# Optimization experiments

Hardware: AMD Instinct MI355X
Metric: run time of the kernel (lower is better)

The kernel has to match this reference:

```python
import jax, jax.numpy as jnp
import numpy as np

AGENT_RADIUS = 0.5
SAFETY_DIST = 0.1
QP_ITERS = 300


def _qp_solve(p, G, h):
    """Batched QP: min_u 0.5 u^T u + p^T u  s.t.  G u <= h  (Q = I).
    Solved in the dual by projected gradient ascent (differentiable, fixed iters).
    p: [B,2], G: [B,m,2], h: [B,m] -> u: [B,2]
    """
    GGt = jnp.einsum('bmi,bni->bmn', G, G)                 # [B,m,m]
    q = jnp.einsum('bmi,bi->bm', G, p) + h                 # [B,m]
    # Lipschitz upper bound per sample (Frobenius norm of GG^T)
    L = jnp.sqrt(jnp.sum(GGt * GGt, axis=(1, 2))) + 1e-6   # [B]
    alpha = (1.0 / L)[:, None]

    def step(lam, _):
        grad = jnp.einsum('bmn,bn->bm', GGt, lam) + q
        lam = jnp.maximum(lam - alpha * grad, 0.0)
        return lam, None

    lam0 = jnp.zeros_like(h)
    lam, _ = jax.lax.scan(step, lam0, None, length=QP_ITERS)
    u = -p - jnp.einsum('bmi,bm->bi', G, lam)
    return u


def setup_inputs() -> dict:
    key = jax.random.key(0)
    ks = jax.random.split(key, 20)
    B, F, H1, H2 = 8192, 8, 1024, 512

    def w(k, i, o):
        return (jax.random.normal(k, (i, o), jnp.float32) / np.sqrt(i)).astype(jnp.float32)

    obs_xy = jax.random.uniform(ks[17], (8, 2), jnp.float32, -10.0, 10.0)
    obs_r = jax.random.uniform(ks[18], (8, 1), jnp.float32, 0.3, 0.8)
    return {
        'x': jax.random.normal(ks[0], (B, F), jnp.float32),
        'mean': 0.1 * jax.random.normal(ks[1], (F,), jnp.float32),
        'std': jax.random.uniform(ks[2], (F,), jnp.float32, 0.5, 1.5),
        'W1': w(ks[3], F, H1), 'b1': jnp.zeros((H1,), jnp.float32),
        'W21': w(ks[4], H1, H2), 'b21': jnp.zeros((H2,), jnp.float32),
        'W22': w(ks[5], H1, H2), 'b22': jnp.zeros((H2,), jnp.float32),
        'W23': w(ks[6], H1, H2), 'b23': jnp.zeros((H2,), jnp.float32),
        'W31': w(ks[7], H2, 2), 'b31': jnp.zeros((2,), jnp.float32),
        'W32': w(ks[8], H2, 2), 'b32': jnp.zeros((2,), jnp.float32),
        'W33': w(ks[9], H2, 1), 'b33': jnp.zeros((1,), jnp.float32),
        'obstacles': jnp.concatenate([obs_xy, obs_r], axis=1),  # [8,3] (x,y,r)
        'sgn': 1,
    }


def reference(x, mean, std, W1, b1, W21, b21, W22, b22, W23, b23,
              W31, b31, W32, b32, W33, b33, obstacles, sgn):
    B = x.shape[0]
    x0 = x * std + mean                                   # un-normalized state [B,8]

    h1 = jax.nn.relu(x @ W1 + b1)
    x21 = jax.nn.relu(h1 @ W21 + b21)
    x22 = jax.nn.relu(h1 @ W22 + b22)
    x23 = jax.nn.relu(h1 @ W23 + b23)
    x31 = x21 @ W31 + b31                                 # QP linear term p [B,2]
    x32 = 4.0 * jax.nn.sigmoid(x22 @ W32 + b32)           # CBF gains p1,p2 [B,2]
    x33 = 4.0 * jax.nn.sigmoid(x23 @ W33 + b33)           # liveness gain (unused, smg off)

    px, py, theta, v = x0[:, 0], x0[:, 1], x0[:, 2], x0[:, 3]
    st, ct = jnp.sin(theta)[:, None], jnp.cos(theta)[:, None]
    vb = v[:, None]

    # static obstacles broadcast to batch + opponent as last obstacle -> [B, m]
    ox = jnp.concatenate([jnp.broadcast_to(obstacles[:, 0][None], (B, obstacles.shape[0])), x0[:, 4:5]], axis=1)
    oy = jnp.concatenate([jnp.broadcast_to(obstacles[:, 1][None], (B, obstacles.shape[0])), x0[:, 5:6]], axis=1)
    orad = jnp.concatenate([jnp.broadcast_to(obstacles[:, 2][None], (B, obstacles.shape[0])),
                            jnp.full((B, 1), AGENT_RADIUS, x0.dtype)], axis=1)

    R = AGENT_RADIUS + orad + SAFETY_DIST
    dx = px[:, None] - ox                                  # [B,m]
    dy = py[:, None] - oy

    barrier = dx * dx + dy * dy - R * R
    barrier_dot = 2.0 * dx * vb * ct + 2.0 * dy * vb * st
    Lf2b = (2.0 * v * v)[:, None]
    LgLfbu1 = -2.0 * dx * vb * st + 2.0 * dy * vb * ct
    LgLfbu2 = 2.0 * dx * ct + 2.0 * dy * st
    G = jnp.stack([-LgLfbu1, -LgLfbu2], axis=-1)           # [B,m,2]
    p1, p2 = x32[:, 0:1], x32[:, 1:2]
    h = Lf2b + (p1 + p2) * barrier_dot + p1 * p2 * barrier # [B,m]

    u = _qp_solve(x31, G, h)                               # [B,2]
    return u
```

## Files before the change

kernel.cpp:

```cpp
#include <hip/hip_runtime.h>
#include <cstdint>
#include <cstddef>

typedef unsigned short u16;
typedef u16   u16x8  __attribute__((ext_vector_type(8)));
typedef u16   u16x4  __attribute__((ext_vector_type(4)));
typedef __bf16 bf16x8 __attribute__((ext_vector_type(8)));
typedef float f32x4  __attribute__((ext_vector_type(4)));
typedef float f32x2  __attribute__((ext_vector_type(2)));

__device__ __forceinline__ u16 f2bf(float f) {
  unsigned int x = __builtin_bit_cast(unsigned int, f);
  x += 0x7fffu + ((x >> 16) & 1u);
  return (u16)(x >> 16);
}

__device__ __forceinline__ void gld_lds16(const u16* g, u16* l) {
  __builtin_amdgcn_global_load_lds(
      (const __attribute__((address_space(1))) unsigned int*)g,
      (__attribute__((address_space(3))) unsigned int*)l, 16, 0, 0);
}

__global__ __launch_bounds__(256) void k_prep(const float* __restrict__ W21,
                                              const float* __restrict__ W22,
                                              u16* __restrict__ Wt,
                                              const float* __restrict__ x,
                                              const float* __restrict__ W1,
                                              const float* __restrict__ b1,
                                              u16* __restrict__ h1,
                                              float* __restrict__ head) {
  __shared__ u16 s[64][65];
  const int b = blockIdx.x;
  if (b < 256) {
    const int mat = b >> 7;
    const int tt  = b & 127;
    const int k0  = (tt >> 3) * 64;
    const int n0  = (tt & 7) * 64;
    const float* W = mat ? W22 : W21;
    const int tx = threadIdx.x & 63;
    const int ty = threadIdx.x >> 6;
#pragma unroll
    for (int i = 0; i < 16; ++i) {
      int r = i * 4 + ty;
      s[r][tx] = f2bf(W[(size_t)(k0 + r) * 512 + n0 + tx]);
    }
    __syncthreads();
    const int nbase = mat * 512 + n0;
#pragma unroll
    for (int i = 0; i < 16; ++i) {
      int r = i * 4 + ty;
      Wt[(size_t)(nbase + r) * 1024 + k0 + tx] = s[tx][r];
    }
  } else {
    const int row0t = (b - 256) * 16;
    if (threadIdx.x < 16)
      *(f32x4*)(head + 4 * (size_t)(row0t + threadIdx.x)) = f32x4{0.f, 0.f, 0.f, 0.f};
    const int c4 = threadIdx.x * 4;
    f32x4 bv = *(const f32x4*)(b1 + c4);
    for (int g = 0; g < 2; ++g) {
      const int row0 = row0t + g * 8;
      f32x4 acc[8];
#pragma unroll
      for (int r = 0; r < 8; ++r) acc[r] = bv;
#pragma unroll
      for (int f = 0; f < 8; ++f) {
        f32x4 wv = *(const f32x4*)(W1 + f * 1024 + c4);
#pragma unroll
        for (int r = 0; r < 8; ++r) {
          float xv = x[(size_t)(row0 + r) * 8 + f];
#pragma unroll
          for (int e = 0; e < 4; ++e) acc[r][e] = fmaf(xv, wv[e], acc[r][e]);
        }
      }
#pragma unroll
      for (int r = 0; r < 8; ++r) {
        u16x4 o;
#pragma unroll
        for (int e = 0; e < 4; ++e) o[e] = f2bf(fmaxf(acc[r][e], 0.f));
        *(u16x4*)(h1 + (size_t)(row0 + r) * 1024 + c4) = o;
      }
    }
  }
}

__global__ __launch_bounds__(256) void k_gemm(const u16* __restrict__ A,
                                              const u16* __restrict__ Bt,
                                              const float* __restrict__ b21,
                                              const float* __restrict__ b22,
                                              const float* __restrict__ W31,
                                              const float* __restrict__ W32,
                                              float* __restrict__ head) {
  constexpr int K  = 1024;
  constexpr int BK = 64;
  constexpr int NT = K / BK;
  __shared__ u16 As[2][128 * 64];
  __shared__ u16 Bs[2][128 * 64];

  const int t    = threadIdx.x;
  const int row0 = blockIdx.x * 128;
  const int col0 = blockIdx.y * 128;
  const int w    = t >> 6;
  const int lane = t & 63;
  const int wr   = w >> 1, wc = w & 1;
  const int lrow = lane & 15;
  const int kq   = lane >> 4;

  const u16* gA[4];
  const u16* gB[4];
  int lo[4];
#pragma unroll
  for (int m = 0; m < 4; ++m) {
    const int s  = t + 256 * m;
    const int gc = (s & 7) ^ ((s >> 3) & 7);
    gA[m] = A  + (size_t)(row0 + (s >> 3)) * K + gc * 8;
    gB[m] = Bt + (size_t)(col0 + (s >> 3)) * K + gc * 8;
    lo[m] = s * 8;
  }
  const int po0 = (((0 * 4) + kq) ^ (lrow & 7)) * 8;
  const int po1 = (((1 * 4) + kq) ^ (lrow & 7)) * 8;

  f32x4 acc[4][4];
#pragma unroll
  for (int i = 0; i < 4; ++i)
#pragma unroll
    for (int j = 0; j < 4; ++j) acc[i][j] = f32x4{0.f, 0.f, 0.f, 0.f};

#pragma unroll
  for (int m = 0; m < 4; ++m) {
    gld_lds16(gA[m], As[0] + lo[m]);
    gld_lds16(gB[m], Bs[0] + lo[m]);
  }

  for (int kt = 0; kt < NT; ++kt) {
    const int cur = kt & 1, nxt = cur ^ 1;
    __syncthreads();

    if (kt + 1 < NT) {
      const int ko = (kt + 1) * BK;
#pragma unroll
      for (int m = 0; m < 4; ++m) {
        gld_lds16(gA[m] + ko, As[nxt] + lo[m]);
        gld_lds16(gB[m] + ko, Bs[nxt] + lo[m]);
      }
    }

#pragma unroll
    for (int s32 = 0; s32 < 2; ++s32) {
      const int po = s32 ? po1 : po0;
      bf16x8 af[4], bfr[4];
#pragma unroll
      for (int i = 0; i < 4; ++i)
        af[i] = __builtin_bit_cast(bf16x8,
            *(const u16x8*)(As[cur] + (wr * 64 + i * 16 + lrow) * 64 + po));
#pragma unroll
      for (int j = 0; j < 4; ++j)
        bfr[j] = __builtin_bit_cast(bf16x8,
            *(const u16x8*)(Bs[cur] + (wc * 64 + j * 16 + lrow) * 64 + po));
#pragma unroll
      for (int i = 0; i < 4; ++i)
#pragma unroll
        for (int j = 0; j < 4; ++j)
          acc[i][j] = __builtin_amdgcn_mfma_f32_16x16x32_bf16(af[i], bfr[j], acc[i][j], 0, 0, 0);
    }
  }

  const bool isX21 = (col0 < 512);
  const float* Wh  = isX21 ? W31 : W32;
  const int   hoff = isX21 ? 0 : 2;

  float hx[16], hy[16];
#pragma unroll
  for (int n = 0; n < 16; ++n) { hx[n] = 0.f; hy[n] = 0.f; }
#pragma unroll
  for (int j = 0; j < 4; ++j) {
    int col  = col0 + wc * 64 + j * 16 + lrow;
    int wcol = col & 511;
    f32x2 wv = *(const f32x2*)(Wh + 2 * wcol);
    float bias = isX21 ? b21[col] : b22[wcol];
#pragma unroll
    for (int i = 0; i < 4; ++i)
#pragma unroll
      for (int rr = 0; rr < 4; ++rr) {
        float v = fmaxf(acc[i][j][rr] + bias, 0.f);
        hx[i * 4 + rr] = fmaf(v, wv[0], hx[i * 4 + rr]);
        hy[i * 4 + rr] = fmaf(v, wv[1], hy[i * 4 + rr]);
      }
  }
#pragma unroll
  for (int m = 1; m <= 8; m <<= 1) {
#pragma unroll
    for (int n = 0; n < 16; ++n) {
      hx[n] += __shfl_xor(hx[n], m, 64);
      hy[n] += __shfl_xor(hy[n], m, 64);
    }
  }
  if (lrow == 0) {
#pragma unroll
    for (int i = 0; i < 4; ++i)
#pragma unroll
      for (int rr = 0; rr < 4; ++rr) {
        int row = row0 + wr * 64 + i * 16 + kq * 4 + rr;
        atomicAdd(head + 4 * (size_t)row + hoff,     hx[i * 4 + rr]);
        atomicAdd(head + 4 * (size_t)row + hoff + 1, hy[i * 4 + rr]);
      }
  }
}

__global__ __launch_bounds__(256) void k_qp(const float* __restrict__ x,
                                            const float* __restrict__ mean_,
                                            const float* __restrict__ std_,
                                            const float* __restrict__ head,
                                            const float* __restrict__ b31,
                                            const float* __restrict__ b32,
                                            const float* __restrict__ obstacles,
                                            float* __restrict__ out) {
  const int r = blockIdx.x * 256 + threadIdx.x;
  f32x4 hd = *(const f32x4*)(head + 4 * (size_t)r);
  float p0  = hd[0] + b31[0];
  float p1v = hd[1] + b31[1];
  float pp1 = 4.f / (1.f + expf(-(hd[2] + b32[0])));
  float pp2 = 4.f / (1.f + expf(-(hd[3] + b32[1])));

  const f32x4* xp = (const f32x4*)(x + (size_t)r * 8);
  f32x4 xa = xp[0], xb = xp[1];
  float px = xa[0] * std_[0] + mean_[0];
  float py = xa[1] * std_[1] + mean_[1];
  float th = xa[2] * std_[2] + mean_[2];
  float v  = xa[3] * std_[3] + mean_[3];
  float ax = xb[0] * std_[4] + mean_[4];
  float ay = xb[1] * std_[5] + mean_[5];
  float st = sinf(th), ct = cosf(th);
  float Lf2b = 2.f * v * v;

  float G0[9], G1[9], q[9];
  float s00 = 0.f, s01 = 0.f, s11 = 0.f;
#pragma unroll
  for (int m = 0; m < 9; ++m) {
    float ox, oy, orad;
    if (m < 8) {
      ox = obstacles[m * 3]; oy = obstacles[m * 3 + 1]; orad = obstacles[m * 3 + 2];
    } else { ox = ax; oy = ay; orad = 0.5f; }
    float R  = 0.6f + orad;
    float dx = px - ox, dy = py - oy;
    float bar  = dx * dx + dy * dy - R * R;
    float dct  = dx * ct + dy * st;
    float bdot = 2.f * v * dct;
    float g0 = 2.f * v * (dx * st - dy * ct);
    float g1 = -2.f * dct;
    float h  = Lf2b + (pp1 + pp2) * bdot + pp1 * pp2 * bar;
    G0[m] = g0; G1[m] = g1;
    q[m] = g0 * p0 + g1 * p1v + h;
    s00 += g0 * g0; s01 += g0 * g1; s11 += g1 * g1;
  }
  float L = sqrtf(s00 * s00 + 2.f * s01 * s01 + s11 * s11) + 1e-6f;
  float alpha = 1.f / L;

  f32x2 G0p[4], G1p[4], qp2[4], lamp[4];
#pragma unroll
  for (int j = 0; j < 4; ++j) {
    G0p[j] = f32x2{G0[j], G0[j + 4]};
    G1p[j] = f32x2{G1[j], G1[j + 4]};
    qp2[j] = f32x2{q[j],  q[j + 4]};
    lamp[j] = f32x2{0.f, 0.f};
  }
  float G08 = G0[8], G18 = G1[8], q8 = q[8], lam8 = 0.f;
  const f32x2 nav = {-alpha, -alpha};
  const f32x2 z2  = {0.f, 0.f};

  for (int it = 0; it < 300; ++it) {
    f32x2 pv0[4], pv1[4];
#pragma unroll
    for (int j = 0; j < 4; ++j) {
      pv0[j] = G0p[j] * lamp[j];
      pv1[j] = G1p[j] * lamp[j];
    }
    float pr08 = G08 * lam8, pr18 = G18 * lam8;
    f32x2 c0 = (pv0[0] + pv0[1]) + (pv0[2] + pv0[3]);
    f32x2 c1 = (pv1[0] + pv1[1]) + (pv1[2] + pv1[3]);
    float t0 = (c0.x + c0.y) + pr08;
    float t1 = (c1.x + c1.y) + pr18;
    f32x2 t0v = {t0, t0}, t1v = {t1, t1};
#pragma unroll
    for (int j = 0; j < 4; ++j) {
      f32x2 g = __builtin_elementwise_fma(G0p[j], t0v,
                __builtin_elementwise_fma(G1p[j], t1v, qp2[j]));
      lamp[j] = __builtin_elementwise_max(
                __builtin_elementwise_fma(nav, g, lamp[j]), z2);
    }
    float g8 = fmaf(G08, t0, fmaf(G18, t1, q8));
    lam8 = fmaxf(fmaf(-alpha, g8, lam8), 0.f);
  }

  float u0 = -p0, u1 = -p1v;
#pragma unroll
  for (int j = 0; j < 4; ++j) {
    u0 = fmaf(-G0p[j].x, lamp[j].x, u0);
    u1 = fmaf(-G1p[j].x, lamp[j].x, u1);
  }
#pragma unroll
  for (int j = 0; j < 4; ++j) {
    u0 = fmaf(-G0p[j].y, lamp[j].y, u0);
    u1 = fmaf(-G1p[j].y, lamp[j].y, u1);
  }
  u0 = fmaf(-G08, lam8, u0);
  u1 = fmaf(-G18, lam8, u1);
  *(f32x2*)(out + 2 * (size_t)r) = f32x2{u0, u1};
}

extern "C" void kernel_launch(void* const* d_in, const int* in_sizes, int n_in,
                              void* d_out, int out_size, void* d_ws, size_t ws_size,
                              hipStream_t stream) {
  const float* x    = (const float*)d_in[0];
  const float* mean_= (const float*)d_in[1];
  const float* std_ = (const float*)d_in[2];
  const float* W1   = (const float*)d_in[3];
  const float* b1   = (const float*)d_in[4];
  const float* W21  = (const float*)d_in[5];
  const float* b21  = (const float*)d_in[6];
  const float* W22  = (const float*)d_in[7];
  const float* b22  = (const float*)d_in[8];
  const float* W31  = (const float*)d_in[11];
  const float* b31  = (const float*)d_in[12];
  const float* W32  = (const float*)d_in[13];
  const float* b32  = (const float*)d_in[14];
  const float* obst = (const float*)d_in[17];
  float* out = (float*)d_out;

  char* ws = (char*)d_ws;
  u16*   Wt   = (u16*)ws;
  u16*   h1   = (u16*)(ws + (size_t)(1 << 21));
  float* head = (float*)(ws + (size_t)(1 << 21) + (size_t)(1 << 24));

  k_prep<<<256 + 512, 256, 0, stream>>>(W21, W22, Wt, x, W1, b1, h1, head);
  k_gemm<<<dim3(64, 8), 256, 0, stream>>>(h1, Wt, b21, b22, W31, W32, head);
  k_qp  <<<32, 256, 0, stream>>>(x, mean_, std_, head, b31, b32, obst, out);
}
```

Before: 159.8 us.

## Fuse first-layer h1 computation into GEMM A-tile production

Computes the 8-to-1024 first layer with ReLU directly inside the GEMM main loop, writing each bf16 A tile into shared memory instead of loading a precomputed h1 buffer. This removes the large h1 global write and read and shrinks the prep kernel to only weight transposition and head zeroing. In exchange, each column block recomputes the same h1 rows, and the per-step FMA work is serialized after the MFMAs, with added register pressure under the new occupancy hint.

```diff
diff --git a/kernel.cpp b/kernel.cpp
--- a/kernel.cpp
+++ b/kernel.cpp
@@ -24,72 +24,44 @@
 __global__ __launch_bounds__(256) void k_prep(const float* __restrict__ W21,
                                               const float* __restrict__ W22,
                                               u16* __restrict__ Wt,
-                                              const float* __restrict__ x,
-                                              const float* __restrict__ W1,
-                                              const float* __restrict__ b1,
-                                              u16* __restrict__ h1,
                                               float* __restrict__ head) {
   __shared__ u16 s[64][65];
   const int b = blockIdx.x;
-  if (b < 256) {
-    const int mat = b >> 7;
-    const int tt  = b & 127;
-    const int k0  = (tt >> 3) * 64;
-    const int n0  = (tt & 7) * 64;
-    const float* W = mat ? W22 : W21;
-    const int tx = threadIdx.x & 63;
-    const int ty = threadIdx.x >> 6;
-#pragma unroll
-    for (int i = 0; i < 16; ++i) {
-      int r = i * 4 + ty;
-      s[r][tx] = f2bf(W[(size_t)(k0 + r) * 512 + n0 + tx]);
-    }
-    __syncthreads();
-    const int nbase = mat * 512 + n0;
-#pragma unroll
-    for (int i = 0; i < 16; ++i) {
-      int r = i * 4 + ty;
-      Wt[(size_t)(nbase + r) * 1024 + k0 + tx] = s[tx][r];
-    }
-  } else {
-    const int row0t = (b - 256) * 16;
-    if (threadIdx.x < 16)
-      *(f32x4*)(head + 4 * (size_t)(row0t + threadIdx.x)) = f32x4{0.f, 0.f, 0.f, 0.f};
-    const int c4 = threadIdx.x * 4;
-    f32x4 bv = *(const f32x4*)(b1 + c4);
-    for (int g = 0; g < 2; ++g) {
-      const int row0 = row0t + g * 8;
-      f32x4 acc[8];
-#pragma unroll
-      for (int r = 0; r < 8; ++r) acc[r] = bv;
-#pragma unroll
-      for (int f = 0; f < 8; ++f) {
-        f32x4 wv = *(const f32x4*)(W1 + f * 1024 + c4);
-#pragma unroll
-        for (int r = 0; r < 8; ++r) {
-          float xv = x[(size_t)(row0 + r) * 8 + f];
-#pragma unroll
-          for (int e = 0; e < 4; ++e) acc[r][e] = fmaf(xv, wv[e], acc[r][e]);
-        }
-      }
-#pragma unroll
-      for (int r = 0; r < 8; ++r) {
-        u16x4 o;
-#pragma unroll
-        for (int e = 0; e < 4; ++e) o[e] = f2bf(fmaxf(acc[r][e], 0.f));
-        *(u16x4*)(h1 + (size_t)(row0 + r) * 1024 + c4) = o;
-      }
-    }
-  }
-}
-
-__global__ __launch_bounds__(256) void k_gemm(const u16* __restrict__ A,
-                                              const u16* __restrict__ Bt,
-                                              const float* __restrict__ b21,
-                                              const float* __restrict__ b22,
-                                              const float* __restrict__ W31,
-                                              const float* __restrict__ W32,
-                                              float* __restrict__ head) {
+  const int t = threadIdx.x;
+  const int gid = b * 256 + t;
+  if (gid < 8192)
+    *(f32x4*)(head + 4 * (size_t)gid) = f32x4{0.f, 0.f, 0.f, 0.f};
+
+  const int mat = b >> 7;
+  const int tt  = b & 127;
+  const int k0  = (tt >> 3) * 64;
+  const int n0  = (tt & 7) * 64;
+  const float* W = mat ? W22 : W21;
+  const int tx = t & 63;
+  const int ty = t >> 6;
+#pragma unroll
+  for (int i = 0; i < 16; ++i) {
+    int r = i * 4 + ty;
+    s[r][tx] = f2bf(W[(size_t)(k0 + r) * 512 + n0 + tx]);
+  }
+  __syncthreads();
+  const int nbase = mat * 512 + n0;
+#pragma unroll
+  for (int i = 0; i < 16; ++i) {
+    int r = i * 4 + ty;
+    Wt[(size_t)(nbase + r) * 1024 + k0 + tx] = s[tx][r];
+  }
+}
+
+__global__ __launch_bounds__(256, 2) void k_gemm(const float* __restrict__ x,
+                                                 const float* __restrict__ W1,
+                                                 const float* __restrict__ b1,
+                                                 const u16* __restrict__ Bt,
+                                                 const float* __restrict__ b21,
+                                                 const float* __restrict__ b22,
+                                                 const float* __restrict__ W31,
+                                                 const float* __restrict__ W32,
+                                                 float* __restrict__ head) {
   constexpr int K  = 1024;
   constexpr int BK = 64;
   constexpr int NT = K / BK;
@@ -105,17 +77,60 @@
   const int lrow = lane & 15;
   const int kq   = lane >> 4;
 
-  const u16* gA[4];
   const u16* gB[4];
-  int lo[4];
+  int loB[4];
 #pragma unroll
   for (int m = 0; m < 4; ++m) {
     const int s  = t + 256 * m;
     const int gc = (s & 7) ^ ((s >> 3) & 7);
-    gA[m] = A  + (size_t)(row0 + (s >> 3)) * K + gc * 8;
-    gB[m] = Bt + (size_t)(col0 + (s >> 3)) * K + gc * 8;
-    lo[m] = s * 8;
-  }
+    gB[m]  = Bt + (size_t)(col0 + (s >> 3)) * K + gc * 8;
+    loB[m] = s * 8;
+  }
+
+  const int g  = t >> 3;
+  const int ch = t & 7;
+  float xr[4][8];
+#pragma unroll
+  for (int rr = 0; rr < 4; ++rr) {
+    f32x4 a = *(const f32x4*)(x + (size_t)(row0 + g * 4 + rr) * 8);
+    f32x4 bq = *(const f32x4*)(x + (size_t)(row0 + g * 4 + rr) * 8 + 4);
+#pragma unroll
+    for (int e = 0; e < 4; ++e) { xr[rr][e] = a[e]; xr[rr][4 + e] = bq[e]; }
+  }
+
+  auto h1_tile = [&](int kt_, u16* dst) {
+    const int k0 = kt_ * BK;
+    f32x4 w1lo[8], w1hi[8];
+#pragma unroll
+    for (int f = 0; f < 8; ++f) {
+      w1lo[f] = *(const f32x4*)(W1 + f * 1024 + k0 + ch * 8);
+      w1hi[f] = *(const f32x4*)(W1 + f * 1024 + k0 + ch * 8 + 4);
+    }
+    const f32x4 blo = *(const f32x4*)(b1 + k0 + ch * 8);
+    const f32x4 bhi = *(const f32x4*)(b1 + k0 + ch * 8 + 4);
+#pragma unroll
+    for (int rr = 0; rr < 4; ++rr) {
+      const int r = g * 4 + rr;
+      f32x4 alo = blo, ahi = bhi;
+#pragma unroll
+      for (int f = 0; f < 8; ++f) {
+        const float xv = xr[rr][f];
+#pragma unroll
+        for (int e = 0; e < 4; ++e) {
+          alo[e] = fmaf(xv, w1lo[f][e], alo[e]);
+          ahi[e] = fmaf(xv, w1hi[f][e], ahi[e]);
+        }
+      }
+      u16x8 o;
+#pragma unroll
+      for (int e = 0; e < 4; ++e) {
+        o[e]     = f2bf(fmaxf(alo[e], 0.f));
+        o[e + 4] = f2bf(fmaxf(ahi[e], 0.f));
+      }
+      *(u16x8*)(dst + r * 64 + (ch ^ (r & 7)) * 8) = o;
+    }
+  };
+
   const int po0 = (((0 * 4) + kq) ^ (lrow & 7)) * 8;
   const int po1 = (((1 * 4) + kq) ^ (lrow & 7)) * 8;
 
@@ -126,10 +141,8 @@
     for (int j = 0; j < 4; ++j) acc[i][j] = f32x4{0.f, 0.f, 0.f, 0.f};
 
 #pragma unroll
-  for (int m = 0; m < 4; ++m) {
-    gld_lds16(gA[m], As[0] + lo[m]);
-    gld_lds16(gB[m], Bs[0] + lo[m]);
-  }
+  for (int m = 0; m < 4; ++m) gld_lds16(gB[m], Bs[0] + loB[m]);
+  h1_tile(0, As[0]);
 
   for (int kt = 0; kt < NT; ++kt) {
     const int cur = kt & 1, nxt = cur ^ 1;
@@ -138,10 +151,7 @@
     if (kt + 1 < NT) {
       const int ko = (kt + 1) * BK;
 #pragma unroll
-      for (int m = 0; m < 4; ++m) {
-        gld_lds16(gA[m] + ko, As[nxt] + lo[m]);
-        gld_lds16(gB[m] + ko, Bs[nxt] + lo[m]);
-      }
+      for (int m = 0; m < 4; ++m) gld_lds16(gB[m] + ko, Bs[nxt] + loB[m]);
     }
 
 #pragma unroll
@@ -162,6 +172,9 @@
         for (int j = 0; j < 4; ++j)
           acc[i][j] = __builtin_amdgcn_mfma_f32_16x16x32_bf16(af[i], bfr[j], acc[i][j], 0, 0, 0);
     }
+
+    if (kt + 1 < NT)
+      h1_tile(kt + 1, As[nxt]);
   }
 
   const bool isX21 = (col0 < 512);
@@ -282,10 +295,10 @@
     f32x2 t0v = {t0, t0}, t1v = {t1, t1};
 #pragma unroll
     for (int j = 0; j < 4; ++j) {
-      f32x2 g = __builtin_elementwise_fma(G0p[j], t0v,
-                __builtin_elementwise_fma(G1p[j], t1v, qp2[j]));
+      f32x2 gg = __builtin_elementwise_fma(G0p[j], t0v,
+                 __builtin_elementwise_fma(G1p[j], t1v, qp2[j]));
       lamp[j] = __builtin_elementwise_max(
-                __builtin_elementwise_fma(nav, g, lamp[j]), z2);
+                __builtin_elementwise_fma(nav, gg, lamp[j]), z2);
     }
     float g8 = fmaf(G08, t0, fmaf(G18, t1, q8));
     lam8 = fmaxf(fmaf(-alpha, g8, lam8), 0.f);
@@ -328,10 +341,9 @@
 
   char* ws = (char*)d_ws;
   u16*   Wt   = (u16*)ws;
-  u16*   h1   = (u16*)(ws + (size_t)(1 << 21));
-  float* head = (float*)(ws + (size_t)(1 << 21) + (size_t)(1 << 24));
-
-  k_prep<<<256 + 512, 256, 0, stream>>>(W21, W22, Wt, x, W1, b1, h1, head);
-  k_gemm<<<dim3(64, 8), 256, 0, stream>>>(h1, Wt, b21, b22, W31, W32, head);
+  float* head = (float*)(ws + (size_t)(1 << 21));
+
+  k_prep<<<256, 256, 0, stream>>>(W21, W22, Wt, head);
+  k_gemm<<<dim3(64, 8), 256, 0, stream>>>(x, W1, b1, Wt, b21, b22, W31, W32, head);
   k_qp  <<<32, 256, 0, stream>>>(x, mean_, std_, head, b31, b32, obst, out);
 }
```

Result: slower. 172.0 us (+7.6%).
